# Performance work log

Hardware: AMD Instinct MI355X
Metric: run time of the kernel (lower is better)

## Reference

```python
import jax, jax.numpy as jnp
import numpy as np
import math

B, S, H = 4, 1024, 1024
E, TOP_K, WINDOW = 4, 2, 64
CONFIGS = [(8, 'standard'), (12, 'standard'), (8, 'linear'), (8, 'local')]
PARAM_NAMES = ['Wq', 'bq', 'Wk', 'bk', 'Wv', 'bv', 'Wo', 'bo']


def setup_inputs() -> dict:
    key = jax.random.key(0)
    ks = jax.random.split(key, 2 + 8 * E)
    d = {}
    d['x'] = jax.random.normal(ks[0], (B, S, H), jnp.float32)
    d['Wg'] = jax.random.normal(ks[1], (H, E), jnp.float32) * 0.02
    i = 2
    for e, (nh, _) in enumerate(CONFIGS):
        hd = H // nh
        pd = nh * hd  # 1020 for nh=12, else 1024
        shapes = [(H, pd), (pd,), (H, pd), (pd,), (H, pd), (pd,), (pd, H), (H,)]
        for nm, shp in zip(PARAM_NAMES, shapes):
            d[f'e{e}_{nm}'] = jax.random.normal(ks[i], shp, jnp.float32) * 0.02
            i += 1
    d['attention_mask'] = jnp.ones((B, S), jnp.int32)
    return d


def _heads(y, nh, hd):
    b, s, _ = y.shape
    return y.reshape(b, s, nh, hd).transpose(0, 2, 1, 3)  # [b, nh, s, hd]


def _attention_expert(x, mask, Wq, bq, Wk, bk, Wv, bv, Wo, bo, nh, atype):
    b, s, _ = x.shape
    hd = Wq.shape[1] // nh
    scale = math.sqrt(hd)
    q = _heads(x @ Wq + bq, nh, hd)
    k = _heads(x @ Wk + bk, nh, hd)
    v = _heads(x @ Wv + bv, nh, hd)
    if atype == 'linear':
        # kernel-trick linear attention; original ignores attention_mask here
        q = jax.nn.elu(q) + 1.0
        k = jax.nn.elu(k) + 1.0
        kv = jnp.einsum('bhsd,bhse->bhde', k, v)
        num = jnp.einsum('bhqd,bhde->bhqe', q, kv)
        den = jnp.einsum('bhqd,bhd->bhq', q, k.sum(axis=2)) + 1e-6
        out = num / den[..., None]
    else:
        scores = jnp.einsum('bhqd,bhkd->bhqk', q, k) / scale
        if atype == 'local':
            idx = jnp.arange(s)
            dist = idx[None, :] - idx[:, None]  # j - i
            local_mask = jnp.abs(dist) <= WINDOW // 2
            scores = jnp.where(local_mask[None, None], scores, -jnp.inf)
        scores = jnp.where(mask[:, None, None, :] == 0, -jnp.inf, scores)
        probs = jax.nn.softmax(scores, axis=-1)
        probs = jnp.where(jnp.isnan(probs), 0.0, probs)  # nan_to_num(nan=0)
        out = jnp.einsum('bhqk,bhkd->bhqd', probs, v)
    out = out.transpose(0, 2, 1, 3).reshape(b, s, -1)
    return out @ Wo + bo


def _forward(x, Wg, eparams, attention_mask):
    b, s, h = x.shape
    # TopKGating (eval mode: no noise). logits -> top_k -> softmax over selected
    logits = x.reshape(-1, h) @ Wg  # [b*s, E]
    top_vals, top_idx = jax.lax.top_k(logits, TOP_K)
    gate_w = jax.nn.softmax(top_vals, axis=-1).reshape(b, s, TOP_K)
    sel = top_idx.reshape(b, s, TOP_K)
    outs = jnp.stack([
        _attention_expert(x, attention_mask, *eparams[e], CONFIGS[e][0], CONFIGS[e][1])
        for e in range(E)
    ], axis=0)  # [E, b, s, h]
    perm = outs.transpose(1, 2, 0, 3)  # [b, s, E, h]
    selected = jnp.take_along_axis(perm, sel[..., None], axis=2)  # [b, s, K, h]
    return (selected * gate_w[..., None]).sum(axis=2)


def reference(x, Wg,
              e0_Wq, e0_bq, e0_Wk, e0_bk, e0_Wv, e0_bv, e0_Wo, e0_bo,
              e1_Wq, e1_bq, e1_Wk, e1_bk, e1_Wv, e1_bv, e1_Wo, e1_bo,
              e2_Wq, e2_bq, e2_Wk, e2_bk, e2_Wv, e2_bv, e2_Wo, e2_bo,
              e3_Wq, e3_bq, e3_Wk, e3_bk, e3_Wv, e3_bv, e3_Wo, e3_bo,
              attention_mask):
    eparams = [
        (e0_Wq, e0_bq, e0_Wk, e0_bk, e0_Wv, e0_bv, e0_Wo, e0_bo),
        (e1_Wq, e1_bq, e1_Wk, e1_bk, e1_Wv, e1_bv, e1_Wo, e1_bo),
        (e2_Wq, e2_bq, e2_Wk, e2_bk, e2_Wv, e2_bv, e2_Wo, e2_bo),
        (e3_Wq, e3_bq, e3_Wk, e3_bk, e3_Wv, e3_bv, e3_Wo, e3_bo),
    ]
    return _forward(x, Wg, eparams, attention_mask)
```

## Files before the change

kernel.cpp:

```cpp
#include <hip/hip_runtime.h>
#include <cmath>

#define B_ 4
#define S_ 1024
#define H_ 1024

typedef short bf16x8 __attribute__((ext_vector_type(8)));
typedef float f32x4 __attribute__((ext_vector_type(4)));
typedef _Float16 half4 __attribute__((ext_vector_type(4)));

__device__ __forceinline__ unsigned short f2bf(float f) {
  unsigned u = __float_as_uint(f);
  u += 0x7fff + ((u >> 16) & 1);
  return (unsigned short)(u >> 16);
}
__device__ __forceinline__ float bf2f(unsigned short h) {
  return __uint_as_float(((unsigned)h) << 16);
}
__device__ __forceinline__ void gld16(const void* g, void* l) {
  __builtin_amdgcn_global_load_lds(
      (const __attribute__((address_space(1))) unsigned int*)g,
      (__attribute__((address_space(3))) unsigned int*)l, 16, 0, 0);
}

__global__ __launch_bounds__(64) void gate_kernel(
    const float* __restrict__ x, const float* __restrict__ Wg,
    float* __restrict__ gw) {
  int t = blockIdx.x;
  int lane = threadIdx.x;
  const float* xr = x + (size_t)t * H_;
  float a0 = 0.f, a1 = 0.f, a2 = 0.f, a3 = 0.f;
  for (int h = lane; h < H_; h += 64) {
    float xv = xr[h];
    const float* wr = Wg + h * 4;
    a0 += xv * wr[0]; a1 += xv * wr[1]; a2 += xv * wr[2]; a3 += xv * wr[3];
  }
  for (int off = 32; off > 0; off >>= 1) {
    a0 += __shfl_down(a0, off);
    a1 += __shfl_down(a1, off);
    a2 += __shfl_down(a2, off);
    a3 += __shfl_down(a3, off);
  }
  if (lane == 0) {
    float v[4] = {a0, a1, a2, a3};
    int i0 = 0; float b0 = v[0];
    for (int e = 1; e < 4; ++e) if (v[e] > b0) { b0 = v[e]; i0 = e; }
    int i1 = -1; float b1 = -INFINITY;
    for (int e = 0; e < 4; ++e) { if (e == i0) continue; if (v[e] > b1) { b1 = v[e]; i1 = e; } }
    float e1v = expf(b1 - b0);
    float w0 = 1.f / (1.f + e1v);
    float w1 = e1v / (1.f + e1v);
    float o[4] = {0.f, 0.f, 0.f, 0.f};
    o[i0] = w0; o[i1] = w1;
    float* g = gw + t * 4;
    g[0] = o[0]; g[1] = o[1]; g[2] = o[2]; g[3] = o[3];
  }
}

__global__ __launch_bounds__(256) void conv_kernel(
    const float* __restrict__ src, unsigned short* __restrict__ dst,
    int nsrc, int ldsrc) {
  int idx = blockIdx.x * 256 + threadIdx.x;
  int m = idx >> 10, c = idx & 1023;
  dst[idx] = (c < nsrc) ? f2bf(src[(size_t)m * ldsrc + c]) : (unsigned short)0;
}

__global__ __launch_bounds__(256) void wtrans4_kernel(
    const float* __restrict__ s0, const float* __restrict__ s1,
    const float* __restrict__ s2, const float* __restrict__ s3,
    unsigned short* __restrict__ d0, unsigned short* __restrict__ d1,
    unsigned short* __restrict__ d2, unsigned short* __restrict__ d3, int pd) {
  __shared__ float tile[32][33];
  int z = blockIdx.z;
  const float* src = (z == 0) ? s0 : (z == 1) ? s1 : (z == 2) ? s2 : s3;
  unsigned short* dst = (z == 0) ? d0 : (z == 1) ? d1 : (z == 2) ? d2 : d3;
  int ksrc = (z < 3) ? 1024 : pd;
  int nsrc = (z < 3) ? pd : 1024;
  int ldsrc = (z < 3) ? pd : 1024;
  int k0 = blockIdx.x * 32, n0 = blockIdx.y * 32;
  int tx = threadIdx.x & 31, ty = threadIdx.x >> 5;
  for (int i = 0; i < 32; i += 8) {
    int k = k0 + ty + i, n = n0 + tx;
    tile[ty + i][tx] = (k < ksrc && n < nsrc) ? src[(size_t)k * ldsrc + n] : 0.f;
  }
  __syncthreads();
  for (int i = 0; i < 32; i += 8) {
    int n = n0 + ty + i, k = k0 + tx;
    dst[(size_t)n * 1024 + k] = f2bf(tile[tx][ty + i]);
  }
}

struct W16 {
  const float* src[16];
  unsigned short* dst[16];
  int pd[4];
};
__global__ __launch_bounds__(256) void wtrans16_kernel(W16 p) {
  __shared__ float tile[32][33];
  int z = blockIdx.z;
  int e = z >> 2, m = z & 3;
  const float* src = p.src[z];
  unsigned short* dst = p.dst[z];
  int pd = p.pd[e];
  int ksrc = (m < 3) ? 1024 : pd;
  int nsrc = (m < 3) ? pd : 1024;
  int ldsrc = (m < 3) ? pd : 1024;
  int k0 = blockIdx.x * 32, n0 = blockIdx.y * 32;
  int tx = threadIdx.x & 31, ty = threadIdx.x >> 5;
  for (int i = 0; i < 32; i += 8) {
    int k = k0 + ty + i, n = n0 + tx;
    tile[ty + i][tx] = (k < ksrc && n < nsrc) ? src[(size_t)k * ldsrc + n] : 0.f;
  }
  __syncthreads();
  for (int i = 0; i < 32; i += 8) {
    int n = n0 + ty + i, k = k0 + tx;
    dst[(size_t)n * 1024 + k] = f2bf(tile[tx][ty + i]);
  }
}

__global__ __launch_bounds__(256) void gemm_mfma(
    const unsigned short* __restrict__ A, const unsigned short* __restrict__ Bt,
    const float* __restrict__ b0, const float* __restrict__ b1,
    const float* __restrict__ b2, void* __restrict__ Cv, int ldc,
    int nact, int elu_ncut, int out_bf16, int mode,
    const float* __restrict__ gw, int expert, int remap,
    int qs_ncut, float qscale) {
  constexpr int K = 1024;
  __shared__ __align__(16) unsigned short As[128 * 32];
  __shared__ __align__(16) unsigned short Bs[128 * 32];
  int tid = threadIdx.x, wave = tid >> 6, lane = tid & 63;
  int quad = lane >> 4, lrow = lane & 15;
  int rw = (wave >> 1) * 64, cw = (wave & 1) * 64;
  int m0 = blockIdx.y * 128, n0 = blockIdx.x * 128;
  int srow = wave * 32 + (lane >> 2);
  int scol = (lane & 3) * 8;
  const unsigned short* gA = A + (size_t)(m0 + srow) * K + scol;
  const unsigned short* gB = Bt + (size_t)(n0 + srow) * K + scol;
  unsigned short* lA = &As[wave * 1024];
  unsigned short* lB = &Bs[wave * 1024];
  f32x4 acc[4][4];
#pragma unroll
  for (int mt = 0; mt < 4; ++mt)
#pragma unroll
    for (int nt = 0; nt < 4; ++nt) acc[mt][nt] = (f32x4){0.f, 0.f, 0.f, 0.f};

  for (int k0 = 0; k0 < K; k0 += 32) {
    gld16(gA + k0, lA);
    gld16(gA + 16 * K + k0, lA + 512);
    gld16(gB + k0, lB);
    gld16(gB + 16 * K + k0, lB + 512);
    __syncthreads();
    bf16x8 af[4], bfr[4];
#pragma unroll
    for (int t = 0; t < 4; ++t) {
      af[t]  = *(const bf16x8*)&As[(rw + t * 16 + lrow) * 32 + quad * 8];
      bfr[t] = *(const bf16x8*)&Bs[(cw + t * 16 + lrow) * 32 + quad * 8];
    }
#pragma unroll
    for (int mt = 0; mt < 4; ++mt)
#pragma unroll
      for (int nt = 0; nt < 4; ++nt)
        acc[mt][nt] = __builtin_amdgcn_mfma_f32_16x16x32_bf16(
            af[mt], bfr[nt], acc[mt][nt], 0, 0, 0);
    __syncthreads();
  }
#pragma unroll
  for (int nt = 0; nt < 4; ++nt) {
    int n = n0 + cw + nt * 16 + lrow;
    int slice = n >> 10, noff = n & 1023;
    if (noff >= nact) continue;
    const float* bp = (slice == 0) ? b0 : (slice == 1) ? b1 : b2;
    float bias = bp[noff];
    bool do_elu = n < elu_ncut;
    bool do_qs = n < qs_ncut;
    int col = n;
    if (remap) {
      int head = (noff * 12337) >> 20;
      col = slice * 1152 + head * 96 + (noff - head * 85);
    }
#pragma unroll
    for (int mt = 0; mt < 4; ++mt) {
      int mb = m0 + rw + mt * 16 + quad * 4;
#pragma unroll
      for (int r = 0; r < 4; ++r) {
        int m = mb + r;
        float val = acc[mt][nt][r] + bias;
        if (do_elu) val = (val > 0.f) ? val + 1.f : expf(val);
        if (do_qs) val *= qscale;
        size_t ci = (size_t)m * ldc + col;
        if (out_bf16) {
          ((unsigned short*)Cv)[ci] = f2bf(val);
        } else {
          float* C = (float*)Cv;
          if (mode == 0) C[ci] = val;
          else {
            float g = gw[m * 4 + expert];
            if (mode == 1) C[ci] = g * val;
            else           C[ci] += g * val;
          }
        }
      }
    }
  }
}

struct QkvP {
  const unsigned short* Bt[4];
  const float* bq[4];
  const float* bk[4];
  const float* bv[4];
  unsigned short* C[4];
  int ldc[4];
  int nact[4];
  int elu_ncut[4];
  int remap[4];
  int qs_ncut[4];
  float qscale[4];
};
__global__ __launch_bounds__(256) void gemm_qkv4(
    const unsigned short* __restrict__ A, QkvP p) {
  constexpr int K = 1024;
  __shared__ __align__(16) unsigned short As[128 * 32];
  __shared__ __align__(16) unsigned short Bs[128 * 32];
  int e = blockIdx.z;
  const unsigned short* Bt = p.Bt[e];
  unsigned short* Cv = p.C[e];
  int ldc = p.ldc[e], nact = p.nact[e], elu_ncut = p.elu_ncut[e];
  int remap = p.remap[e], qs_ncut = p.qs_ncut[e];
  float qscale = p.qscale[e];
  int tid = threadIdx.x, wave = tid >> 6, lane = tid & 63;
  int quad = lane >> 4, lrow = lane & 15;
  int rw = (wave >> 1) * 64, cw = (wave & 1) * 64;
  int m0 = blockIdx.y * 128, n0 = blockIdx.x * 128;
  int srow = wave * 32 + (lane >> 2);
  int scol = (lane & 3) * 8;
  const unsigned short* gA = A + (size_t)(m0 + srow) * K + scol;
  const unsigned short* gB = Bt + (size_t)(n0 + srow) * K + scol;
  unsigned short* lA = &As[wave * 1024];
  unsigned short* lB = &Bs[wave * 1024];
  f32x4 acc[4][4];
#pragma unroll
  for (int mt = 0; mt < 4; ++mt)
#pragma unroll
    for (int nt = 0; nt < 4; ++nt) acc[mt][nt] = (f32x4){0.f, 0.f, 0.f, 0.f};

  for (int k0 = 0; k0 < K; k0 += 32) {
    gld16(gA + k0, lA);
    gld16(gA + 16 * K + k0, lA + 512);
    gld16(gB + k0, lB);
    gld16(gB + 16 * K + k0, lB + 512);
    __syncthreads();
    bf16x8 af[4], bfr[4];
#pragma unroll
    for (int t = 0; t < 4; ++t) {
      af[t]  = *(const bf16x8*)&As[(rw + t * 16 + lrow) * 32 + quad * 8];
      bfr[t] = *(const bf16x8*)&Bs[(cw + t * 16 + lrow) * 32 + quad * 8];
    }
#pragma unroll
    for (int mt = 0; mt < 4; ++mt)
#pragma unroll
      for (int nt = 0; nt < 4; ++nt)
        acc[mt][nt] = __builtin_amdgcn_mfma_f32_16x16x32_bf16(
            af[mt], bfr[nt], acc[mt][nt], 0, 0, 0);
    __syncthreads();
  }
#pragma unroll
  for (int nt = 0; nt < 4; ++nt) {
    int n = n0 + cw + nt * 16 + lrow;
    int slice = n >> 10, noff = n & 1023;
    if (noff >= nact) continue;
    const float* bp = (slice == 0) ? p.bq[e] : (slice == 1) ? p.bk[e] : p.bv[e];
    float bias = bp[noff];
    bool do_elu = n < elu_ncut;
    bool do_qs = n < qs_ncut;
    int col = n;
    if (remap) {
      int head = (noff * 12337) >> 20;
      col = slice * 1152 + head * 96 + (noff - head * 85);
    }
#pragma unroll
    for (int mt = 0; mt < 4; ++mt) {
      int mb = m0 + rw + mt * 16 + quad * 4;
#pragma unroll
      for (int r = 0; r < 4; ++r) {
        int m = mb + r;
        float val = acc[mt][nt][r] + bias;
        if (do_elu) val = (val > 0.f) ? val + 1.f : expf(val);
        if (do_qs) val *= qscale;
        Cv[(size_t)m * ldc + col] = f2bf(val);
      }
    }
  }
}

struct OutP {
  const unsigned short* A[4];
  const unsigned short* B[4];
  const float* bias[4];
};

__global__ __launch_bounds__(256) void gemm_out4(
    OutP p, const float* __restrict__ gw, float* __restrict__ part) {
  constexpr int K = 1024;
  __shared__ __align__(16) unsigned short As[128 * 32];
  __shared__ __align__(16) unsigned short Bs[128 * 32];
  int e = blockIdx.z;
  const unsigned short* A = p.A[e];
  const unsigned short* Bt = p.B[e];
  const float* bp = p.bias[e];
  float* C = part + (size_t)e * (4096ull * 1024ull);
  int tid = threadIdx.x, wave = tid >> 6, lane = tid & 63;
  int quad = lane >> 4, lrow = lane & 15;
  int rw = (wave >> 1) * 64, cw = (wave & 1) * 64;
  int m0 = blockIdx.y * 128, n0 = blockIdx.x * 128;
  int srow = wave * 32 + (lane >> 2);
  int scol = (lane & 3) * 8;
  const unsigned short* gA = A + (size_t)(m0 + srow) * K + scol;
  const unsigned short* gB = Bt + (size_t)(n0 + srow) * K + scol;
  unsigned short* lA = &As[wave * 1024];
  unsigned short* lB = &Bs[wave * 1024];
  f32x4 acc[4][4];
#pragma unroll
  for (int mt = 0; mt < 4; ++mt)
#pragma unroll
    for (int nt = 0; nt < 4; ++nt) acc[mt][nt] = (f32x4){0.f, 0.f, 0.f, 0.f};

  for (int k0 = 0; k0 < K; k0 += 32) {
    gld16(gA + k0, lA);
    gld16(gA + 16 * K + k0, lA + 512);
    gld16(gB + k0, lB);
    gld16(gB + 16 * K + k0, lB + 512);
    __syncthreads();
    bf16x8 af[4], bfr[4];
#pragma unroll
    for (int t = 0; t < 4; ++t) {
      af[t]  = *(const bf16x8*)&As[(rw + t * 16 + lrow) * 32 + quad * 8];
      bfr[t] = *(const bf16x8*)&Bs[(cw + t * 16 + lrow) * 32 + quad * 8];
    }
#pragma unroll
    for (int mt = 0; mt < 4; ++mt)
#pragma unroll
      for (int nt = 0; nt < 4; ++nt)
        acc[mt][nt] = __builtin_amdgcn_mfma_f32_16x16x32_bf16(
            af[mt], bfr[nt], acc[mt][nt], 0, 0, 0);
    __syncthreads();
  }
#pragma unroll
  for (int nt = 0; nt < 4; ++nt) {
    int n = n0 + cw + nt * 16 + lrow;
    float bias = bp[n];
#pragma unroll
    for (int mt = 0; mt < 4; ++mt) {
      int mb = m0 + rw + mt * 16 + quad * 4;
#pragma unroll
      for (int r = 0; r < 4; ++r) {
        int m = mb + r;
        float g = gw[m * 4 + e];
        C[(size_t)m * 1024 + n] = g * (acc[mt][nt][r] + bias);
      }
    }
  }
}

__global__ __launch_bounds__(256) void reduce4(
    const float* __restrict__ part, float* __restrict__ out) {
  constexpr size_t N = 4096ull * 1024ull;
  size_t idx = ((size_t)blockIdx.x * 256 + threadIdx.x) * 4;
  f32x4 a0 = *(const f32x4*)(part + idx);
  f32x4 a1 = *(const f32x4*)(part + idx + N);
  f32x4 a2 = *(const f32x4*)(part + idx + 2 * N);
  f32x4 a3 = *(const f32x4*)(part + idx + 3 * N);
  f32x4 s;
#pragma unroll
  for (int j = 0; j < 4; ++j) {
    float t = a0[j];
    t += a1[j]; t += a2[j]; t += a3[j];
    s[j] = t;
  }
  *(f32x4*)(out + idx) = s;
}

__global__ __launch_bounds__(256) void padzero(
    unsigned short* __restrict__ qkv1, unsigned short* __restrict__ aob1) {
  int idx = blockIdx.x * 256 + threadIdx.x;
  int m = idx / 396, r = idx % 396;
  int slice = r / 132, r2 = r % 132;
  int head = r2 / 11, c = 85 + r2 % 11;
  qkv1[(size_t)m * 3456 + slice * 1152 + head * 96 + c] = 0;
  if (idx < 4096 * 4) {
    int mm = idx >> 2, cc = 1020 + (idx & 3);
    aob1[(size_t)mm * 1024 + cc] = 0;
  }
}

template <int HD, bool LOCAL>
__device__ __forceinline__ void attn_body(
    char* smem,
    const unsigned short* __restrict__ q, const unsigned short* __restrict__ k,
    const unsigned short* __restrict__ v, const int* __restrict__ amask,
    unsigned short* __restrict__ ao, int ldq, int h) {
  constexpr int HDP = (HD + 31) & ~31;
  constexpr int DCH = HDP / 32;
  constexpr int NDT = HDP / 16;
  constexpr int NCH = HDP / 8;
  constexpr int QT = 256, KT = 64;
  constexpr int KLD = HDP + 8;
  constexpr int VLD = KT + 4;
  constexpr int W2 = 32;
  constexpr int KSZ = KT * KLD;
  constexpr int VSZ = HDP * VLD;
  unsigned short* Ks = (unsigned short*)smem;
  _Float16* Vt = (_Float16*)(smem + 2 * KSZ * 2);
  unsigned long long* amq =
      (unsigned long long*)(smem + 2 * KSZ * 2 + 2 * VSZ * 2);
  int tid = threadIdx.x, wave = tid >> 6, lane = tid & 63;
  int quad = lane >> 4, l15 = lane & 15;
  int q0 = blockIdx.x * QT, b = blockIdx.z;
  size_t baseq = ((size_t)b * S_) * ldq + (size_t)h * HDP;
  size_t baseo = ((size_t)b * S_) * H_ + (size_t)h * HD;

  {
    unsigned long long bb0 = __ballot(amask[b * S_ + wave * 128 + lane] != 0);
    unsigned long long bb1 = __ballot(amask[b * S_ + wave * 128 + 64 + lane] != 0);
    if (lane == 0) { amq[wave * 2] = bb0; amq[wave * 2 + 1] = bb1; }
  }

  int qrow[2];
  bf16x8 qf[2][DCH];
#pragma unroll
  for (int g = 0; g < 2; ++g) {
    qrow[g] = q0 + wave * 32 + g * 16 + l15;
#pragma unroll
    for (int c = 0; c < DCH; ++c)
#pragma unroll
      for (int j = 0; j < 8; ++j) {
        int d = c * 32 + quad * 8 + j;
        qf[g][c][j] =
            (d < HD) ? (short)q[baseq + (size_t)qrow[g] * ldq + d] : (short)0;
      }
  }

  int jlo = 0, jhi = S_;
  if (LOCAL) {
    jlo = q0 - W2; if (jlo < 0) jlo = 0; jlo &= ~(KT - 1);
    jhi = q0 + QT + W2; if (jhi > S_) jhi = S_;
  }

  int skey = tid & 63, sc8a = tid >> 6, sc8b = 8 + (tid >> 6);
  bool sactb = sc8b < NCH;
  const unsigned short* kg = k + baseq + (size_t)skey * ldq;
  const unsigned short* vg = v + baseq + (size_t)skey * ldq;
  bf16x8 kra = {}, krb = {}, vra = {}, vrb = {};
  {
    size_t o = (size_t)jlo * ldq;
    kra = *(const bf16x8*)(kg + o + sc8a * 8);
    vra = *(const bf16x8*)(vg + o + sc8a * 8);
    if (sactb) {
      krb = *(const bf16x8*)(kg + o + sc8b * 8);
      vrb = *(const bf16x8*)(vg + o + sc8b * 8);
    }
  }

  {
    *(bf16x8*)&Ks[skey * KLD + sc8a * 8] = kra;
#pragma unroll
    for (int j = 0; j < 8; ++j)
      Vt[(sc8a * 8 + j) * VLD + skey] = (_Float16)bf2f((unsigned short)vra[j]);
    if (sactb) {
      *(bf16x8*)&Ks[skey * KLD + sc8b * 8] = krb;
#pragma unroll
      for (int j = 0; j < 8; ++j)
        Vt[(sc8b * 8 + j) * VLD + skey] = (_Float16)bf2f((unsigned short)vrb[j]);
    }
  }
  int cur = 0;
  __syncthreads();

  float m_run[2] = {-1e30f, -1e30f}, l_run[2] = {0.f, 0.f};
  f32x4 accd[2][NDT];
#pragma unroll
  for (int g = 0; g < 2; ++g)
#pragma unroll
    for (int dt = 0; dt < NDT; ++dt) accd[g][dt] = (f32x4){0.f, 0.f, 0.f, 0.f};

  for (int j0 = jlo; j0 < jhi; j0 += KT) {
    int jn = j0 + KT;
    if (jn < jhi) {
      size_t o = (size_t)jn * ldq;
      kra = *(const bf16x8*)(kg + o + sc8a * 8);
      vra = *(const bf16x8*)(vg + o + sc8a * 8);
      if (sactb) {
        krb = *(const bf16x8*)(kg + o + sc8b * 8);
        vrb = *(const bf16x8*)(vg + o + sc8b * 8);
      }
    }
    const unsigned short* KsR = Ks + cur * KSZ;
    const _Float16* VtR = Vt + cur * VSZ;
    f32x4 sf[2][4];
#pragma unroll
    for (int kt = 0; kt < 4; ++kt) {
      sf[0][kt] = (f32x4){0.f, 0.f, 0.f, 0.f};
      sf[1][kt] = (f32x4){0.f, 0.f, 0.f, 0.f};
#pragma unroll
      for (int c = 0; c < DCH; ++c) {
        bf16x8 kf = *(const bf16x8*)&KsR[(kt * 16 + l15) * KLD + c * 32 + quad * 8];
        sf[0][kt] = __builtin_amdgcn_mfma_f32_16x16x32_bf16(kf, qf[0][c], sf[0][kt], 0, 0, 0);
        sf[1][kt] = __builtin_amdgcn_mfma_f32_16x16x32_bf16(kf, qf[1][c], sf[1][kt], 0, 0, 0);
      }
    }
    unsigned long long mb = amq[j0 >> 6];
    unsigned mw[2] = {(unsigned)mb, (unsigned)(mb >> 32)};
    float pvv[2][4][4];
    float mx[2] = {-1e30f, -1e30f};
#pragma unroll
    for (int kt = 0; kt < 4; ++kt) {
      unsigned word = mw[kt >> 1];
      int sh = (kt & 1) * 16 + quad * 4;
#pragma unroll
      for (int r = 0; r < 4; ++r) {
        bool okm = (word >> (sh + r)) & 1;
#pragma unroll
        for (int g = 0; g < 2; ++g) {
          bool ok = okm;
          if (LOCAL) {
            int dj = (j0 + kt * 16 + quad * 4 + r) - qrow[g];
            ok = ok && (dj <= W2) && (dj >= -W2);
          }
          float s = ok ? sf[g][kt][r] : -1e30f;
          pvv[g][kt][r] = s;
          mx[g] = fmaxf(mx[g], s);
        }
      }
    }
    half4 pf[2][4];
    float aR[2][4];
#pragma unroll
    for (int g = 0; g < 2; ++g) {
      float mxg = fmaxf(mx[g], __shfl_xor(mx[g], 16));
      mxg = fmaxf(mxg, __shfl_xor(mxg, 32));
      float m_new = fmaxf(m_run[g], mxg);
      float psum = 0.f;
#pragma unroll
      for (int kt = 0; kt < 4; ++kt)
#pragma unroll
        for (int r = 0; r < 4; ++r) {
          float s = pvv[g][kt][r];
          float p = (s > -1e29f) ? __builtin_amdgcn_exp2f(s - m_new) : 0.f;
          pvv[g][kt][r] = p;
          psum += p;
        }
      psum += __shfl_xor(psum, 16);
      psum += __shfl_xor(psum, 32);
      float alpha = __builtin_amdgcn_exp2f(m_run[g] - m_new);
      m_run[g] = m_new;
      l_run[g] = l_run[g] * alpha + psum;
#pragma unroll
      for (int r = 0; r < 4; ++r)
        aR[g][r] = __shfl(alpha, (lane & 48) | (quad * 4 + r));
#pragma unroll
      for (int dt = 0; dt < NDT; ++dt)
#pragma unroll
        for (int r = 0; r < 4; ++r) accd[g][dt][r] *= aR[g][r];
#pragma unroll
      for (int kt = 0; kt < 4; ++kt)
#pragma unroll
        for (int r = 0; r < 4; ++r) pf[g][kt][r] = (_Float16)pvv[g][kt][r];
    }
    if (jn < jhi) {
      unsigned short* KsW = Ks + (cur ^ 1) * KSZ;
      _Float16* VtW = Vt + (cur ^ 1) * VSZ;
      *(bf16x8*)&KsW[skey * KLD + sc8a * 8] = kra;
#pragma unroll
      for (int j = 0; j < 8; ++j)
        VtW[(sc8a * 8 + j) * VLD + skey] = (_Float16)bf2f((unsigned short)vra[j]);
      if (sactb) {
        *(bf16x8*)&KsW[skey * KLD + sc8b * 8] = krb;
#pragma unroll
        for (int j = 0; j < 8; ++j)
          VtW[(sc8b * 8 + j) * VLD + skey] = (_Float16)bf2f((unsigned short)vrb[j]);
      }
    }
#pragma unroll
    for (int dt = 0; dt < NDT; ++dt)
#pragma unroll
      for (int kt = 0; kt < 4; ++kt) {
        half4 vf = *(const half4*)&VtR[(dt * 16 + l15) * VLD + kt * 16 + quad * 4];
        accd[0][dt] = __builtin_amdgcn_mfma_f32_16x16x16f16(pf[0][kt], vf, accd[0][dt], 0, 0, 0);
        accd[1][dt] = __builtin_amdgcn_mfma_f32_16x16x16f16(pf[1][kt], vf, accd[1][dt], 0, 0, 0);
      }
    __syncthreads();
    cur ^= 1;
  }
#pragma unroll
  for (int g = 0; g < 2; ++g) {
    float linv = (l_run[g] > 0.f) ? 1.f / l_run[g] : 0.f;
    float lR[4];
#pragma unroll
    for (int r = 0; r < 4; ++r)
      lR[r] = __shfl(linv, (lane & 48) | (quad * 4 + r));
#pragma unroll
    for (int dt = 0; dt < NDT; ++dt) {
      int d = dt * 16 + l15;
      if (d >= HD) continue;
#pragma unroll
      for (int r = 0; r < 4; ++r) {
        int row = q0 + wave * 32 + g * 16 + quad * 4 + r;
        ao[baseo + (size_t)row * H_ + d] = f2bf(accd[g][dt][r] * lR[r]);
      }
    }
  }
}

template <int HD, bool LOCAL>
__global__ __launch_bounds__(512) void attn_mfma3(
    const unsigned short* __restrict__ q, const unsigned short* __restrict__ k,
    const unsigned short* __restrict__ v, const int* __restrict__ amask,
    unsigned short* __restrict__ ao, int ldq) {
  constexpr int HDP = (HD + 31) & ~31;
  __shared__ __align__(16) char smem[2 * 64 * (HDP + 8) * 2 + 2 * HDP * 68 * 2 + 128];
  attn_body<HD, LOCAL>(smem, q, k, v, amask, ao, ldq, blockIdx.y);
}

__global__ __launch_bounds__(512) void attn_mega(
    const unsigned short* __restrict__ qkv0,
    const unsigned short* __restrict__ qkv1,
    const unsigned short* __restrict__ qkv3, const int* __restrict__ amask,
    unsigned short* __restrict__ ao0, unsigned short* __restrict__ ao1,
    unsigned short* __restrict__ ao3) {
  __shared__ __align__(16) char smem[69760];
  int y = blockIdx.y;
  if (y < 8)
    attn_body<128, false>(smem, qkv0, qkv0 + 1024, qkv0 + 2048, amask, ao0,
                          3072, y);
  else if (y < 20)
    attn_body<85, false>(smem, qkv1, qkv1 + 1152, qkv1 + 2304, amask, ao1,
                         3456, y - 8);
  else
    attn_body<128, true>(smem, qkv3, qkv3 + 1024, qkv3 + 2048, amask, ao3,
                         3072, y - 20);
}

#define NSPLIT 4
__global__ __launch_bounds__(256) void linkv_mfma(
    const unsigned short* __restrict__ k, const unsigned short* __restrict__ v,
    float* __restrict__ kvp, float* __restrict__ ksump, int ld) {
  constexpr int HD = 128;
  constexpr int TLD = 34;
  __shared__ __align__(16) unsigned short Kt[HD * TLD];
  __shared__ __align__(16) unsigned short Vt[HD * TLD];
  int h = blockIdx.x, b = blockIdx.y, split = blockIdx.z;
  int bh = b * 8 + h;
  int tid = threadIdx.x, wave = tid >> 6, lane = tid & 63;
  int quad = lane >> 4, l15 = lane & 15;
  int rw = (wave >> 1) * 64, cw = (wave & 1) * 64;
  size_t base = ((size_t)b * S_) * ld + (size_t)h * HD;
  int s_begin = split * (S_ / NSPLIT);

  f32x4 acc[4][4];
#pragma unroll
  for (int mt = 0; mt < 4; ++mt)
#pragma unroll
    for (int nt = 0; nt < 4; ++nt) acc[mt][nt] = (f32x4){0.f, 0.f, 0.f, 0.f};
  float ksacc = 0.f;
  int myd = tid & 127, half = tid >> 7;

  for (int c0 = 0; c0 < S_ / NSPLIT; c0 += 32) {
    for (int idx = tid; idx < 32 * HD; idx += 256) {
      int d = idx & 127, s = idx >> 7;
      size_t g = base + (size_t)(s_begin + c0 + s) * ld + d;
      Kt[d * TLD + s] = k[g];
      Vt[d * TLD + s] = v[g];
    }
    __syncthreads();
    bf16x8 af[4], bf[4];
#pragma unroll
    for (int t = 0; t < 4; ++t) {
      af[t] = *(const bf16x8*)&Vt[(rw + t * 16 + l15) * TLD + quad * 8];
      bf[t] = *(const bf16x8*)&Kt[(cw + t * 16 + l15) * TLD + quad * 8];
    }
#pragma unroll
    for (int mt = 0; mt < 4; ++mt)
#pragma unroll
      for (int nt = 0; nt < 4; ++nt)
        acc[mt][nt] = __builtin_amdgcn_mfma_f32_16x16x32_bf16(
            af[mt], bf[nt], acc[mt][nt], 0, 0, 0);
#pragma unroll
    for (int s = 0; s < 16; ++s)
      ksacc += bf2f(Kt[myd * TLD + half * 16 + s]);
    __syncthreads();
  }
  float* red = (float*)Kt;
  if (half == 1) red[myd] = ksacc;
  __syncthreads();
  if (half == 0)
    ksump[((size_t)split * 32 + bh) * HD + myd] = ksacc + red[myd];
  float* kvo = kvp + ((size_t)split * 32 + bh) * (HD * HD);
#pragma unroll
  for (int mt = 0; mt < 4; ++mt)
#pragma unroll
    for (int nt = 0; nt < 4; ++nt) {
      int dk = cw + nt * 16 + l15;
#pragma unroll
      for (int r = 0; r < 4; ++r) {
        int dv = rw + mt * 16 + quad * 4 + r;
        kvo[(size_t)dv * HD + dk] = acc[mt][nt][r];
      }
    }
}

__global__ __launch_bounds__(256) void linkv_reduce(
    const float* __restrict__ kvp, const float* __restrict__ ksump,
    unsigned short* __restrict__ kvb, float* __restrict__ ksum) {
  int idx = blockIdx.x * 256 + threadIdx.x;
  float s = 0.f;
#pragma unroll
  for (int p = 0; p < NSPLIT; ++p) s += kvp[(size_t)p * (32 * 128 * 128) + idx];
  kvb[idx] = f2bf(s);
  if (idx < 32 * 128) {
    float t = 0.f;
#pragma unroll
    for (int p = 0; p < NSPLIT; ++p) t += ksump[(size_t)p * (32 * 128) + idx];
    ksum[idx] = t;
  }
}

__global__ __launch_bounds__(256) void linattn_mfma(
    const unsigned short* __restrict__ q, const unsigned short* __restrict__ kvT,
    const float* __restrict__ ksum, unsigned short* __restrict__ ao, int ldq) {
  constexpr int KLD = 136;
  __shared__ __align__(16) unsigned short Ks[128 * KLD];
  __shared__ float ksL[128];
  int tid = threadIdx.x, wave = tid >> 6, lane = tid & 63;
  int quad = lane >> 4, l15 = lane & 15;
  int rw = (wave >> 1) * 64, cw = (wave & 1) * 64;
  int q0 = blockIdx.x * 128, h = blockIdx.y, b = blockIdx.z;
  int bh = b * 8 + h;
  size_t baseq = ((size_t)b * S_) * ldq + (size_t)h * 128;
  size_t baseo = ((size_t)b * S_) * H_ + (size_t)h * 128;
  const unsigned short* kvg = kvT + (size_t)bh * (128 * 128);
  for (int idx = tid; idx < 128 * 16; idx += 256) {
    int e = idx >> 4, c = idx & 15;
    *(bf16x8*)&Ks[e * KLD + c * 8] = *(const bf16x8*)&kvg[e * 128 + c * 8];
  }
  if (tid < 128) ksL[tid] = ksum[(size_t)bh * 128 + tid];
  bf16x8 qf[4][4];
#pragma unroll
  for (int mt = 0; mt < 4; ++mt) {
    const unsigned short* qr = q + baseq + (size_t)(q0 + rw + mt * 16 + l15) * ldq;
#pragma unroll
    for (int kc = 0; kc < 4; ++kc)
      qf[mt][kc] = *(const bf16x8*)&qr[kc * 32 + quad * 8];
  }
  __syncthreads();
  f32x4 acc[4][4];
#pragma unroll
  for (int mt = 0; mt < 4; ++mt)
#pragma unroll
    for (int nt = 0; nt < 4; ++nt) acc[mt][nt] = (f32x4){0.f, 0.f, 0.f, 0.f};
#pragma unroll
  for (int kc = 0; kc < 4; ++kc) {
    bf16x8 bf[4];
#pragma unroll
    for (int nt = 0; nt < 4; ++nt)
      bf[nt] = *(const bf16x8*)&Ks[(cw + nt * 16 + l15) * KLD + kc * 32 + quad * 8];
#pragma unroll
    for (int mt = 0; mt < 4; ++mt)
#pragma unroll
      for (int nt = 0; nt < 4; ++nt)
        acc[mt][nt] = __builtin_amdgcn_mfma_f32_16x16x32_bf16(
            qf[mt][kc], bf[nt], acc[mt][nt], 0, 0, 0);
  }
  float den[4];
#pragma unroll
  for (int mt = 0; mt < 4; ++mt) {
    float s = 0.f;
#pragma unroll
    for (int kc = 0; kc < 4; ++kc)
#pragma unroll
      for (int j = 0; j < 8; ++j)
        s += bf2f((unsigned short)qf[mt][kc][j]) * ksL[kc * 32 + quad * 8 + j];
    s += __shfl_xor(s, 16);
    s += __shfl_xor(s, 32);
    den[mt] = s;
  }
#pragma unroll
  for (int mt = 0; mt < 4; ++mt)
#pragma unroll
    for (int r = 0; r < 4; ++r) {
      float dv = __shfl(den[mt], (lane & 48) | (quad * 4 + r));
      float inv = 1.f / (dv + 1e-6f);
      int row = q0 + rw + mt * 16 + quad * 4 + r;
#pragma unroll
      for (int nt = 0; nt < 4; ++nt) {
        int col = cw + nt * 16 + l15;
        ao[baseo + (size_t)row * H_ + col] = f2bf(acc[mt][nt][r] * inv);
      }
    }
}

extern "C" void kernel_launch(void* const* d_in, const int* in_sizes, int n_in,
                              void* d_out, int out_size, void* d_ws, size_t ws_size,
                              hipStream_t stream) {
  const float* x = (const float*)d_in[0];
  const float* Wg = (const float*)d_in[1];
  const int* amask = (const int*)d_in[34];
  float* out = (float*)d_out;
  char* ws = (char*)d_ws;
  const size_t MiB = 1ull << 20;
  const int nhs[4] = {8, 12, 8, 8};
  const float LOG2E = 1.4426950408889634f;

  if (ws_size >= 157 * MiB) {
    float* gw = (float*)ws;
    float* ksum = (float*)(ws + (64ull << 10));
    unsigned short* kvb = (unsigned short*)(ws + 1 * MiB);
    unsigned short* xb = (unsigned short*)(ws + 4 * MiB);
    float* kvp = (float*)(ws + 4 * MiB);
    float* ksump = (float*)(ws + 12 * MiB);
    unsigned short* woT[4];
    for (int e = 0; e < 4; ++e)
      woT[e] = (unsigned short*)(ws + (18 + 2 * e) * MiB);
    const size_t qkvOff[4] = {26 * MiB, 50 * MiB, 77 * MiB, 101 * MiB};
    unsigned short* qkvE[4];
    for (int e = 0; e < 4; ++e) qkvE[e] = (unsigned short*)(ws + qkvOff[e]);
    float* part = (float*)(ws + 26 * MiB);
    unsigned short* aobE[4];
    for (int e = 0; e < 4; ++e)
      aobE[e] = (unsigned short*)(ws + (125 + 8 * e) * MiB);
    unsigned short* qkvT4 = (unsigned short*)(ws + 125 * MiB);

    conv_kernel<<<16384, 256, 0, stream>>>(x, xb, 1024, 1024);
    gate_kernel<<<4096, 64, 0, stream>>>(x, Wg, gw);

    W16 w;
    for (int e = 0; e < 4; ++e) {
      w.pd[e] = nhs[e] * (H_ / nhs[e]);
      for (int m = 0; m < 3; ++m) {
        w.src[e * 4 + m] = (const float*)d_in[2 + 8 * e + 2 * m];
        w.dst[e * 4 + m] = qkvT4 + (size_t)(e * 3 + m) * (1 << 20);
      }
      w.src[e * 4 + 3] = (const float*)d_in[2 + 8 * e + 6];
      w.dst[e * 4 + 3] = woT[e];
    }
    wtrans16_kernel<<<dim3(32, 32, 16), 256, 0, stream>>>(w);

    QkvP qp;
    for (int e = 0; e < 4; ++e) {
      int hd = H_ / nhs[e];
      int pd = nhs[e] * hd;
      qp.Bt[e] = qkvT4 + (size_t)(e * 3) * (1 << 20);
      qp.bq[e] = (const float*)d_in[2 + 8 * e + 1];
      qp.bk[e] = (const float*)d_in[2 + 8 * e + 3];
      qp.bv[e] = (const float*)d_in[2 + 8 * e + 5];
      qp.C[e] = qkvE[e];
      qp.ldc[e] = (e == 1) ? 3456 : 3072;
      qp.nact[e] = (pd == 1020) ? 1020 : 1024;
      qp.elu_ncut[e] = (e == 2) ? 2048 : 0;
      qp.remap[e] = (e == 1) ? 1 : 0;
      qp.qs_ncut[e] = (e == 2) ? 0 : 1024;
      qp.qscale[e] = LOG2E / sqrtf((float)hd);
    }
    gemm_qkv4<<<dim3(24, 32, 4), 256, 0, stream>>>(xb, qp);

    padzero<<<6336, 256, 0, stream>>>(qkvE[1], aobE[1]);

    linkv_mfma<<<dim3(8, B_, NSPLIT), 256, 0, stream>>>(
        qkvE[2] + 1024, qkvE[2] + 2048, kvp, ksump, 3072);
    linkv_reduce<<<(32 * 128 * 128) / 256, 256, 0, stream>>>(kvp, ksump, kvb, ksum);
    linattn_mfma<<<dim3(S_ / 128, 8, B_), 256, 0, stream>>>(
        qkvE[2], kvb, ksum, aobE[2], 3072);

    attn_mega<<<dim3(S_ / 256, 28, B_), 512, 0, stream>>>(
        qkvE[0], qkvE[1], qkvE[3], amask, aobE[0], aobE[1], aobE[3]);

    OutP p;
    for (int e = 0; e < 4; ++e) {
      p.A[e] = aobE[e];
      p.B[e] = woT[e];
      p.bias[e] = (const float*)d_in[2 + 8 * e + 7];
    }
    gemm_out4<<<dim3(8, 32, 4), 256, 0, stream>>>(p, gw, part);
    reduce4<<<4096, 256, 0, stream>>>(part, out);
    return;
  }

  float* gw            = (float*)(ws + 0);
  unsigned short* kvb  = (unsigned short*)(ws + (1ull << 20));
  float* ksum          = (float*)(ws + (3ull << 20) + (1ull << 19));
  unsigned short* xb   = (unsigned short*)(ws + (4ull << 20));
  unsigned short* qkvT = (unsigned short*)(ws + (12ull << 20));
  unsigned short* woT  = (unsigned short*)(ws + (18ull << 20));
  unsigned short* qkv  = (unsigned short*)(ws + (20ull << 20));
  unsigned short* aob  = (unsigned short*)(ws + (49ull << 20));
  float* kvp           = (float*)(ws + (57ull << 20));
  float* ksump         = (float*)(ws + (73ull << 20));

  conv_kernel<<<16384, 256, 0, stream>>>(x, xb, 1024, 1024);
  gate_kernel<<<4096, 64, 0, stream>>>(x, Wg, gw);

  for (int e = 0; e < 4; ++e) {
    const float* Wq = (const float*)d_in[2 + 8 * e + 0];
    const float* bq = (const float*)d_in[2 + 8 * e + 1];
    const float* Wk = (const float*)d_in[2 + 8 * e + 2];
    const float* bk = (const float*)d_in[2 + 8 * e + 3];
    const float* Wv = (const float*)d_in[2 + 8 * e + 4];
    const float* bv = (const float*)d_in[2 + 8 * e + 5];
    const float* Wo = (const float*)d_in[2 + 8 * e + 6];
    const float* bo = (const float*)d_in[2 + 8 * e + 7];
    int nh = nhs[e];
    int hd = H_ / nh;
    int pd = nh * hd;
    int ldqkv = (e == 1) ? 3456 : 3072;
    int qs_ncut = (e == 2) ? 0 : 1024;
    float qscale = LOG2E / sqrtf((float)hd);

    wtrans4_kernel<<<dim3(32, 32, 4), 256, 0, stream>>>(
        Wq, Wk, Wv, Wo, qkvT, qkvT + (1 << 20), qkvT + (2 << 20), woT, pd);

    gemm_mfma<<<dim3(24, 32), 256, 0, stream>>>(
        xb, qkvT, bq, bk, bv, qkv, ldqkv,
        (pd == 1020) ? 1020 : 1024, (e == 2) ? 2048 : 0, 1, 0, nullptr, 0,
        (e == 1) ? 1 : 0, qs_ncut, qscale);

    if (e == 2) {
      const unsigned short* qb = qkv;
      const unsigned short* kb = qkv + 1024;
      const unsigned short* vb = qkv + 2048;
      linkv_mfma<<<dim3(8, B_, NSPLIT), 256, 0, stream>>>(kb, vb, kvp, ksump, 3072);
      linkv_reduce<<<(32 * 128 * 128) / 256, 256, 0, stream>>>(kvp, ksump, kvb, ksum);
      linattn_mfma<<<dim3(S_ / 128, 8, B_), 256, 0, stream>>>(qb, kvb, ksum, aob, 3072);
    } else if (e == 1) {
      attn_mfma3<85, false><<<dim3(S_ / 256, 12, B_), 512, 0, stream>>>(
          qkv, qkv + 1152, qkv + 2304, amask, aob, 3456);
    } else if (e == 3) {
      attn_mfma3<128, true><<<dim3(S_ / 256, 8, B_), 512, 0, stream>>>(
          qkv, qkv + 1024, qkv + 2048, amask, aob, 3072);
    } else {
      attn_mfma3<128, false><<<dim3(S_ / 256, 8, B_), 512, 0, stream>>>(
          qkv, qkv + 1024, qkv + 2048, amask, aob, 3072);
    }

    gemm_mfma<<<dim3(8, 32), 256, 0, stream>>>(
        aob, woT, bo, bo, bo, out, 1024, 1024, 0, 0, (e == 0) ? 1 : 2, gw, e, 0,
        0, 1.0f);
  }
}
```

Before: 578.0 us.

## Fuse gate with bf16 conversion, deepen GEMM K-step, merge linear KV into attn_mega

Several separate changes. The gate kernel now also writes the bf16 copy of x, which removes a separate conversion pass over the input. Both projection GEMMs load a 64-wide K slice per barrier instead of 32, halving the number of synchronisations at the cost of doubling LDS use. The linear-attention KV accumulation moves into extra grid rows of the attention megakernel, with two 256-thread sub-blocks per 512-thread block, so it runs concurrently with softmax attention instead of as its own launch.

```diff
diff --git a/kernel.cpp b/kernel.cpp
--- a/kernel.cpp
+++ b/kernel.cpp
@@ -32,6 +32,42 @@
   float a0 = 0.f, a1 = 0.f, a2 = 0.f, a3 = 0.f;
   for (int h = lane; h < H_; h += 64) {
     float xv = xr[h];
+    const float* wr = Wg + h * 4;
+    a0 += xv * wr[0]; a1 += xv * wr[1]; a2 += xv * wr[2]; a3 += xv * wr[3];
+  }
+  for (int off = 32; off > 0; off >>= 1) {
+    a0 += __shfl_down(a0, off);
+    a1 += __shfl_down(a1, off);
+    a2 += __shfl_down(a2, off);
+    a3 += __shfl_down(a3, off);
+  }
+  if (lane == 0) {
+    float v[4] = {a0, a1, a2, a3};
+    int i0 = 0; float b0 = v[0];
+    for (int e = 1; e < 4; ++e) if (v[e] > b0) { b0 = v[e]; i0 = e; }
+    int i1 = -1; float b1 = -INFINITY;
+    for (int e = 0; e < 4; ++e) { if (e == i0) continue; if (v[e] > b1) { b1 = v[e]; i1 = e; } }
+    float e1v = expf(b1 - b0);
+    float w0 = 1.f / (1.f + e1v);
+    float w1 = e1v / (1.f + e1v);
+    float o[4] = {0.f, 0.f, 0.f, 0.f};
+    o[i0] = w0; o[i1] = w1;
+    float* g = gw + t * 4;
+    g[0] = o[0]; g[1] = o[1]; g[2] = o[2]; g[3] = o[3];
+  }
+}
+
+__global__ __launch_bounds__(64) void gate_conv_kernel(
+    const float* __restrict__ x, const float* __restrict__ Wg,
+    float* __restrict__ gw, unsigned short* __restrict__ xb) {
+  int t = blockIdx.x;
+  int lane = threadIdx.x;
+  const float* xr = x + (size_t)t * H_;
+  unsigned short* xbr = xb + (size_t)t * H_;
+  float a0 = 0.f, a1 = 0.f, a2 = 0.f, a3 = 0.f;
+  for (int h = lane; h < H_; h += 64) {
+    float xv = xr[h];
+    xbr[h] = f2bf(xv);
     const float* wr = Wg + h * 4;
     a0 += xv * wr[0]; a1 += xv * wr[1]; a2 += xv * wr[2]; a3 += xv * wr[3];
   }
@@ -220,8 +256,8 @@
 __global__ __launch_bounds__(256) void gemm_qkv4(
     const unsigned short* __restrict__ A, QkvP p) {
   constexpr int K = 1024;
-  __shared__ __align__(16) unsigned short As[128 * 32];
-  __shared__ __align__(16) unsigned short Bs[128 * 32];
+  __shared__ __align__(16) unsigned short As[2 * 128 * 32];
+  __shared__ __align__(16) unsigned short Bs[2 * 128 * 32];
   int e = blockIdx.z;
   const unsigned short* Bt = p.Bt[e];
   unsigned short* Cv = p.C[e];
@@ -244,24 +280,33 @@
 #pragma unroll
     for (int nt = 0; nt < 4; ++nt) acc[mt][nt] = (f32x4){0.f, 0.f, 0.f, 0.f};
 
-  for (int k0 = 0; k0 < K; k0 += 32) {
+  for (int k0 = 0; k0 < K; k0 += 64) {
     gld16(gA + k0, lA);
     gld16(gA + 16 * K + k0, lA + 512);
+    gld16(gA + k0 + 32, lA + 4096);
+    gld16(gA + 16 * K + k0 + 32, lA + 4096 + 512);
     gld16(gB + k0, lB);
     gld16(gB + 16 * K + k0, lB + 512);
+    gld16(gB + k0 + 32, lB + 4096);
+    gld16(gB + 16 * K + k0 + 32, lB + 4096 + 512);
     __syncthreads();
-    bf16x8 af[4], bfr[4];
-#pragma unroll
-    for (int t = 0; t < 4; ++t) {
-      af[t]  = *(const bf16x8*)&As[(rw + t * 16 + lrow) * 32 + quad * 8];
-      bfr[t] = *(const bf16x8*)&Bs[(cw + t * 16 + lrow) * 32 + quad * 8];
-    }
-#pragma unroll
-    for (int mt = 0; mt < 4; ++mt)
-#pragma unroll
-      for (int nt = 0; nt < 4; ++nt)
-        acc[mt][nt] = __builtin_amdgcn_mfma_f32_16x16x32_bf16(
-            af[mt], bfr[nt], acc[mt][nt], 0, 0, 0);
+#pragma unroll
+    for (int kk = 0; kk < 2; ++kk) {
+      const unsigned short* Ap = As + kk * 4096;
+      const unsigned short* Bp = Bs + kk * 4096;
+      bf16x8 af[4], bfr[4];
+#pragma unroll
+      for (int t = 0; t < 4; ++t) {
+        af[t]  = *(const bf16x8*)&Ap[(rw + t * 16 + lrow) * 32 + quad * 8];
+        bfr[t] = *(const bf16x8*)&Bp[(cw + t * 16 + lrow) * 32 + quad * 8];
+      }
+#pragma unroll
+      for (int mt = 0; mt < 4; ++mt)
+#pragma unroll
+        for (int nt = 0; nt < 4; ++nt)
+          acc[mt][nt] = __builtin_amdgcn_mfma_f32_16x16x32_bf16(
+              af[mt], bfr[nt], acc[mt][nt], 0, 0, 0);
+    }
     __syncthreads();
   }
 #pragma unroll
@@ -302,8 +347,8 @@
 __global__ __launch_bounds__(256) void gemm_out4(
     OutP p, const float* __restrict__ gw, float* __restrict__ part) {
   constexpr int K = 1024;
-  __shared__ __align__(16) unsigned short As[128 * 32];
-  __shared__ __align__(16) unsigned short Bs[128 * 32];
+  __shared__ __align__(16) unsigned short As[2 * 128 * 32];
+  __shared__ __align__(16) unsigned short Bs[2 * 128 * 32];
   int e = blockIdx.z;
   const unsigned short* A = p.A[e];
   const unsigned short* Bt = p.B[e];
@@ -325,24 +370,33 @@
 #pragma unroll
     for (int nt = 0; nt < 4; ++nt) acc[mt][nt] = (f32x4){0.f, 0.f, 0.f, 0.f};
 
-  for (int k0 = 0; k0 < K; k0 += 32) {
+  for (int k0 = 0; k0 < K; k0 += 64) {
     gld16(gA + k0, lA);
     gld16(gA + 16 * K + k0, lA + 512);
+    gld16(gA + k0 + 32, lA + 4096);
+    gld16(gA + 16 * K + k0 + 32, lA + 4096 + 512);
     gld16(gB + k0, lB);
     gld16(gB + 16 * K + k0, lB + 512);
+    gld16(gB + k0 + 32, lB + 4096);
+    gld16(gB + 16 * K + k0 + 32, lB + 4096 + 512);
     __syncthreads();
-    bf16x8 af[4], bfr[4];
-#pragma unroll
-    for (int t = 0; t < 4; ++t) {
-      af[t]  = *(const bf16x8*)&As[(rw + t * 16 + lrow) * 32 + quad * 8];
-      bfr[t] = *(const bf16x8*)&Bs[(cw + t * 16 + lrow) * 32 + quad * 8];
-    }
-#pragma unroll
-    for (int mt = 0; mt < 4; ++mt)
-#pragma unroll
-      for (int nt = 0; nt < 4; ++nt)
-        acc[mt][nt] = __builtin_amdgcn_mfma_f32_16x16x32_bf16(
-            af[mt], bfr[nt], acc[mt][nt], 0, 0, 0);
+#pragma unroll
+    for (int kk = 0; kk < 2; ++kk) {
+      const unsigned short* Ap = As + kk * 4096;
+      const unsigned short* Bp = Bs + kk * 4096;
+      bf16x8 af[4], bfr[4];
+#pragma unroll
+      for (int t = 0; t < 4; ++t) {
+        af[t]  = *(const bf16x8*)&Ap[(rw + t * 16 + lrow) * 32 + quad * 8];
+        bfr[t] = *(const bf16x8*)&Bp[(cw + t * 16 + lrow) * 32 + quad * 8];
+      }
+#pragma unroll
+      for (int mt = 0; mt < 4; ++mt)
+#pragma unroll
+        for (int nt = 0; nt < 4; ++nt)
+          acc[mt][nt] = __builtin_amdgcn_mfma_f32_16x16x32_bf16(
+              af[mt], bfr[nt], acc[mt][nt], 0, 0, 0);
+    }
     __syncthreads();
   }
 #pragma unroll
@@ -621,12 +675,90 @@
   attn_body<HD, LOCAL>(smem, q, k, v, amask, ao, ldq, blockIdx.y);
 }
 
+#define NSPLIT 4
+__device__ __forceinline__ void linkv_body(
+    char* smemi, const unsigned short* __restrict__ k,
+    const unsigned short* __restrict__ v, float* __restrict__ kvp,
+    float* __restrict__ ksump, int ld, int h, int b, int split, int tid) {
+  constexpr int HD = 128;
+  constexpr int TLD = 34;
+  unsigned short* Kt = (unsigned short*)smemi;
+  unsigned short* Vt = Kt + HD * TLD;
+  int bh = b * 8 + h;
+  int wave = tid >> 6, lane = tid & 63;
+  int quad = lane >> 4, l15 = lane & 15;
+  int rw = (wave >> 1) * 64, cw = (wave & 1) * 64;
+  size_t base = ((size_t)b * S_) * ld + (size_t)h * HD;
+  int s_begin = split * (S_ / NSPLIT);
+
+  f32x4 acc[4][4];
+#pragma unroll
+  for (int mt = 0; mt < 4; ++mt)
+#pragma unroll
+    for (int nt = 0; nt < 4; ++nt) acc[mt][nt] = (f32x4){0.f, 0.f, 0.f, 0.f};
+  float ksacc = 0.f;
+  int myd = tid & 127, half = tid >> 7;
+
+  for (int c0 = 0; c0 < S_ / NSPLIT; c0 += 32) {
+    for (int idx = tid; idx < 32 * HD; idx += 256) {
+      int d = idx & 127, s = idx >> 7;
+      size_t g = base + (size_t)(s_begin + c0 + s) * ld + d;
+      Kt[d * TLD + s] = k[g];
+      Vt[d * TLD + s] = v[g];
+    }
+    __syncthreads();
+    bf16x8 af[4], bf[4];
+#pragma unroll
+    for (int t = 0; t < 4; ++t) {
+      af[t] = *(const bf16x8*)&Vt[(rw + t * 16 + l15) * TLD + quad * 8];
+      bf[t] = *(const bf16x8*)&Kt[(cw + t * 16 + l15) * TLD + quad * 8];
+    }
+#pragma unroll
+    for (int mt = 0; mt < 4; ++mt)
+#pragma unroll
+      for (int nt = 0; nt < 4; ++nt)
+        acc[mt][nt] = __builtin_amdgcn_mfma_f32_16x16x32_bf16(
+            af[mt], bf[nt], acc[mt][nt], 0, 0, 0);
+#pragma unroll
+    for (int s = 0; s < 16; ++s)
+      ksacc += bf2f(Kt[myd * TLD + half * 16 + s]);
+    __syncthreads();
+  }
+  float* red = (float*)Kt;
+  if (half == 1) red[myd] = ksacc;
+  __syncthreads();
+  if (half == 0)
+    ksump[((size_t)split * 32 + bh) * HD + myd] = ksacc + red[myd];
+  float* kvo = kvp + ((size_t)split * 32 + bh) * (HD * HD);
+#pragma unroll
+  for (int mt = 0; mt < 4; ++mt)
+#pragma unroll
+    for (int nt = 0; nt < 4; ++nt) {
+      int dk = cw + nt * 16 + l15;
+#pragma unroll
+      for (int r = 0; r < 4; ++r) {
+        int dv = rw + mt * 16 + quad * 4 + r;
+        kvo[(size_t)dv * HD + dk] = acc[mt][nt][r];
+      }
+    }
+}
+
+__global__ __launch_bounds__(256) void linkv_mfma(
+    const unsigned short* __restrict__ k, const unsigned short* __restrict__ v,
+    float* __restrict__ kvp, float* __restrict__ ksump, int ld) {
+  __shared__ __align__(16) char smemi[17408];
+  linkv_body(smemi, k, v, kvp, ksump, ld, blockIdx.x, blockIdx.y, blockIdx.z,
+             threadIdx.x);
+}
+
 __global__ __launch_bounds__(512) void attn_mega(
     const unsigned short* __restrict__ qkv0,
     const unsigned short* __restrict__ qkv1,
+    const unsigned short* __restrict__ qkv2,
     const unsigned short* __restrict__ qkv3, const int* __restrict__ amask,
     unsigned short* __restrict__ ao0, unsigned short* __restrict__ ao1,
-    unsigned short* __restrict__ ao3) {
+    unsigned short* __restrict__ ao3,
+    float* __restrict__ kvp, float* __restrict__ ksump) {
   __shared__ __align__(16) char smem[69760];
   int y = blockIdx.y;
   if (y < 8)
@@ -635,77 +767,15 @@
   else if (y < 20)
     attn_body<85, false>(smem, qkv1, qkv1 + 1152, qkv1 + 2304, amask, ao1,
                          3456, y - 8);
-  else
+  else if (y < 28)
     attn_body<128, true>(smem, qkv3, qkv3 + 1024, qkv3 + 2048, amask, ao3,
                          3072, y - 20);
-}
-
-#define NSPLIT 4
-__global__ __launch_bounds__(256) void linkv_mfma(
-    const unsigned short* __restrict__ k, const unsigned short* __restrict__ v,
-    float* __restrict__ kvp, float* __restrict__ ksump, int ld) {
-  constexpr int HD = 128;
-  constexpr int TLD = 34;
-  __shared__ __align__(16) unsigned short Kt[HD * TLD];
-  __shared__ __align__(16) unsigned short Vt[HD * TLD];
-  int h = blockIdx.x, b = blockIdx.y, split = blockIdx.z;
-  int bh = b * 8 + h;
-  int tid = threadIdx.x, wave = tid >> 6, lane = tid & 63;
-  int quad = lane >> 4, l15 = lane & 15;
-  int rw = (wave >> 1) * 64, cw = (wave & 1) * 64;
-  size_t base = ((size_t)b * S_) * ld + (size_t)h * HD;
-  int s_begin = split * (S_ / NSPLIT);
-
-  f32x4 acc[4][4];
-#pragma unroll
-  for (int mt = 0; mt < 4; ++mt)
-#pragma unroll
-    for (int nt = 0; nt < 4; ++nt) acc[mt][nt] = (f32x4){0.f, 0.f, 0.f, 0.f};
-  float ksacc = 0.f;
-  int myd = tid & 127, half = tid >> 7;
-
-  for (int c0 = 0; c0 < S_ / NSPLIT; c0 += 32) {
-    for (int idx = tid; idx < 32 * HD; idx += 256) {
-      int d = idx & 127, s = idx >> 7;
-      size_t g = base + (size_t)(s_begin + c0 + s) * ld + d;
-      Kt[d * TLD + s] = k[g];
-      Vt[d * TLD + s] = v[g];
-    }
-    __syncthreads();
-    bf16x8 af[4], bf[4];
-#pragma unroll
-    for (int t = 0; t < 4; ++t) {
-      af[t] = *(const bf16x8*)&Vt[(rw + t * 16 + l15) * TLD + quad * 8];
-      bf[t] = *(const bf16x8*)&Kt[(cw + t * 16 + l15) * TLD + quad * 8];
-    }
-#pragma unroll
-    for (int mt = 0; mt < 4; ++mt)
-#pragma unroll
-      for (int nt = 0; nt < 4; ++nt)
-        acc[mt][nt] = __builtin_amdgcn_mfma_f32_16x16x32_bf16(
-            af[mt], bf[nt], acc[mt][nt], 0, 0, 0);
-#pragma unroll
-    for (int s = 0; s < 16; ++s)
-      ksacc += bf2f(Kt[myd * TLD + half * 16 + s]);
-    __syncthreads();
-  }
-  float* red = (float*)Kt;
-  if (half == 1) red[myd] = ksacc;
-  __syncthreads();
-  if (half == 0)
-    ksump[((size_t)split * 32 + bh) * HD + myd] = ksacc + red[myd];
-  float* kvo = kvp + ((size_t)split * 32 + bh) * (HD * HD);
-#pragma unroll
-  for (int mt = 0; mt < 4; ++mt)
-#pragma unroll
-    for (int nt = 0; nt < 4; ++nt) {
-      int dk = cw + nt * 16 + l15;
-#pragma unroll
-      for (int r = 0; r < 4; ++r) {
-        int dv = rw + mt * 16 + quad * 4 + r;
-        kvo[(size_t)dv * HD + dk] = acc[mt][nt][r];
-      }
-    }
+  else {
+    int sub = threadIdx.x >> 8, stid = threadIdx.x & 255;
+    int idx = (y - 28) * 8 + blockIdx.x * 2 + sub;
+    linkv_body(smem + sub * 17408, qkv2 + 1024, qkv2 + 2048, kvp, ksump, 3072,
+               idx & 7, blockIdx.z, idx >> 3, stid);
+  }
 }
 
 __global__ __launch_bounds__(256) void linkv_reduce(
@@ -829,8 +899,7 @@
       aobE[e] = (unsigned short*)(ws + (125 + 8 * e) * MiB);
     unsigned short* qkvT4 = (unsigned short*)(ws + 125 * MiB);
 
-    conv_kernel<<<16384, 256, 0, stream>>>(x, xb, 1024, 1024);
-    gate_kernel<<<4096, 64, 0, stream>>>(x, Wg, gw);
+    gate_conv_kernel<<<4096, 64, 0, stream>>>(x, Wg, gw, xb);
 
     W16 w;
     for (int e = 0; e < 4; ++e) {
@@ -864,14 +933,13 @@
 
     padzero<<<6336, 256, 0, stream>>>(qkvE[1], aobE[1]);
 
-    linkv_mfma<<<dim3(8, B_, NSPLIT), 256, 0, stream>>>(
-        qkvE[2] + 1024, qkvE[2] + 2048, kvp, ksump, 3072);
+    attn_mega<<<dim3(S_ / 256, 32, B_), 512, 0, stream>>>(
+        qkvE[0], qkvE[1], qkvE[2], qkvE[3], amask, aobE[0], aobE[1], aobE[3],
+        kvp, ksump);
+
     linkv_reduce<<<(32 * 128 * 128) / 256, 256, 0, stream>>>(kvp, ksump, kvb, ksum);
     linattn_mfma<<<dim3(S_ / 128, 8, B_), 256, 0, stream>>>(
         qkvE[2], kvb, ksum, aobE[2], 3072);
-
-    attn_mega<<<dim3(S_ / 256, 28, B_), 512, 0, stream>>>(
-        qkvE[0], qkvE[1], qkvE[3], amask, aobE[0], aobE[1], aobE[3]);
 
     OutP p;
     for (int e = 0; e < 4; ++e) {
```

Result: faster. 527.8 us (-8.7%).
